# Kernel optimization log

Hardware: AMD Instinct MI355X
Metric: run time of the kernel (lower is better)

Reference implementation:

```python
import jax, jax.numpy as jnp
import numpy as np

B, L, IMG_DIM, D, H = 256, 64, 2048, 1024, 8
DH = D // H
NEG = -1e30
LN_EPS = 1e-5
BN_EPS = 1e-5
RESW = 0.5
K = 2


def setup_inputs() -> dict:
    key = jax.random.key(0)
    ks = jax.random.split(key, 24)
    n = jax.random.normal
    inp = {
        "images": n(ks[0], (B, L, IMG_DIM), dtype=jnp.float32),
        "image_lengths": jax.random.randint(ks[1], (B,), 2, L + 1).astype(jnp.int32),
        # FC_MLP: Linear(2048->512) -> BN -> ReLU -> Linear(512->1024)
        "fc1_w": n(ks[2], (512, IMG_DIM)) * 0.02,
        "fc1_b": jnp.zeros((512,)),
        "bn_g": jnp.ones((512,)),
        "bn_b": jnp.zeros((512,)),
        "bn_m": jnp.zeros((512,)),
        "bn_v": jnp.ones((512,)),
        "fc2_w": n(ks[3], (D, 512)) * 0.02,
        "fc2_b": jnp.zeros((D,)),
        # MHA
        "in_w": n(ks[4], (3 * D, D)) * 0.02,
        "in_b": jnp.zeros((3 * D,)),
        "out_w": n(ks[5], (D, D)) * 0.02,
        "out_b": jnp.zeros((D,)),
        "ln1_g": jnp.ones((D,)),
        "ln1_b": jnp.zeros((D,)),
        # FFN (dim_feedforward = embed_size = 1024)
        "ff1_w": n(ks[6], (D, D)) * 0.02,
        "ff1_b": jnp.zeros((D,)),
        "ff2_w": n(ks[7], (D, D)) * 0.02,
        "ff2_b": jnp.zeros((D,)),
        "ln2_g": jnp.ones((D,)),
        "ln2_b": jnp.zeros((D,)),
    }
    return inp


def _layernorm(x, g, b):
    mu = x.mean(-1, keepdims=True)
    var = ((x - mu) ** 2).mean(-1, keepdims=True)
    return (x - mu) * jax.lax.rsqrt(var + LN_EPS) * g + b


def reference(images, image_lengths, fc1_w, fc1_b, bn_g, bn_b, bn_m, bn_v,
              fc2_w, fc2_b, in_w, in_b, out_w, out_b, ln1_g, ln1_b,
              ff1_w, ff1_b, ff2_w, ff2_b, ln2_g, ln2_b):
    lengths = image_lengths
    valid = jnp.arange(L)[None, :] < lengths[:, None]          # (B, L) True=valid

    # FC_MLP (BN in eval mode with running stats)
    h = images @ fc1_w.T + fc1_b
    h = (h - bn_m) * jax.lax.rsqrt(bn_v + BN_EPS) * bn_g + bn_b
    h = jax.nn.relu(h)
    emb = h @ fc2_w.T + fc2_b                                   # (B, L, D)

    # Maxk_Pooling_Variable: top-k over valid tokens, mean of top-k, per feature
    masked = jnp.where(valid[:, :, None], emb, NEG)             # (B, L, D)
    topk, _ = jax.lax.top_k(masked.transpose(0, 2, 1), K)       # (B, D, K)
    emb_res = topk.mean(-1)                                     # (B, D)

    # TransformerEncoderLayer (post-norm, relu, dropout=0) with key padding mask
    qkv = emb @ in_w.T + in_b
    q, k, v = jnp.split(qkv, 3, axis=-1)
    q = q.reshape(B, L, H, DH)
    k = k.reshape(B, L, H, DH)
    v = v.reshape(B, L, H, DH)
    scores = jnp.einsum("bqhd,bkhd->bhqk", q, k) / np.sqrt(DH)
    scores = scores + jnp.where(valid, 0.0, NEG)[:, None, None, :]
    attn = jax.nn.softmax(scores, axis=-1)
    ctx = jnp.einsum("bhqk,bkhd->bqhd", attn, v).reshape(B, L, D)
    ctx = ctx @ out_w.T + out_b
    x = _layernorm(emb + ctx, ln1_g, ln1_b)
    ff = jax.nn.relu(x @ ff1_w.T + ff1_b) @ ff2_w.T + ff2_b
    x = _layernorm(x + ff, ln2_g, ln2_b)                        # (B, L, D)

    # Avg_Pooling_Variable: mean over first lengths[i] tokens
    avg = (x * valid[:, :, None]).sum(1) / lengths[:, None].astype(x.dtype)

    out = RESW * emb_res + (1.0 - RESW) * avg                   # (B, D)
    norm = jnp.sqrt((out ** 2).sum(-1, keepdims=True)) + 1e-8
    return out / norm
```

## Files before the change

kernel.cpp:

```cpp
#include <hip/hip_runtime.h>
#include <stdint.h>
#include <stddef.h>


typedef short s16x8 __attribute__((ext_vector_type(8)));
typedef short s16x4 __attribute__((ext_vector_type(4)));
typedef float f32x4 __attribute__((ext_vector_type(4)));

#define LN_EPSF 1e-5f
#define BN_EPSF 1e-5f

__device__ __forceinline__ short f2bf(float f) {
  union { float f; uint32_t u; } x; x.f = f;
  uint32_t r = x.u + 0x7fffu + ((x.u >> 16) & 1u);
  return (short)(r >> 16);
}
__device__ __forceinline__ float bf2f(short s) {
  union { uint32_t u; float f; } x; x.u = ((uint32_t)(uint16_t)s) << 16;
  return x.f;
}

typedef const __attribute__((address_space(1))) short glb_s16_t;
typedef __attribute__((address_space(3))) short lds_s16_t;

__device__ __forceinline__ void stage16(const short* g, short* l) {
  __builtin_amdgcn_global_load_lds((glb_s16_t*)g, (lds_s16_t*)l, 16, 0, 0);
}

__device__ __forceinline__ int swz(int off) {
  return off ^ (((off >> 7) & 3) << 4);
}

enum { EPI_PLAIN = 0, EPI_FF1 = 3, EPI_RES = 4 };

__global__ __launch_bounds__(256)
void prefix_kernel(const int* __restrict__ lens, int* __restrict__ cum,
                   int* __restrict__ hdr, int* __restrict__ tokmap) {
  __shared__ int wsum[4];
  __shared__ int sc[256];
  __shared__ int mcpad;
  const int tid = threadIdx.x, lane = tid & 63, wave = tid >> 6;
  const int mylen = lens[tid];
  int v = mylen;
#pragma unroll
  for (int o = 1; o < 64; o <<= 1) {
    int t = __shfl_up(v, o);
    if (lane >= o) v += t;
  }
  if (lane == 63) wsum[wave] = v;
  __syncthreads();
  int add = 0;
#pragma unroll
  for (int w2 = 0; w2 < 4; ++w2) if (w2 < wave) add += wsum[w2];
  const int incl = v + add;
  const int excl = incl - mylen;
  cum[tid] = excl;
  sc[tid] = excl;
  if (tid == 255) {
    hdr[0] = incl;
    mcpad  = (incl + 255) & ~255;
    hdr[1] = mcpad;
  }
  __syncthreads();
  for (int l = 0; l < mylen; ++l) tokmap[excl + l] = tid * 64 + l;
  const int mc = sc[255] + lens[255];
  for (int i = mc + tid; i < mcpad; i += 256) tokmap[i] = 0;
}

struct CvtArgs { const float* src[6]; short* dst[6]; int n4[6]; };

__global__ __launch_bounds__(256)
void cvt_gather_kernel(const float* __restrict__ img,
                       const int* __restrict__ tokmap,
                       const int* __restrict__ hdr, short* __restrict__ out,
                       CvtArgs a) {
  const int n4 = hdr[1] << 9;
  const int stride = gridDim.x * 256;
  for (int i = blockIdx.x * 256 + threadIdx.x; i < n4; i += stride) {
    const int row = i >> 9, col = i & 511;
    float4 v = ((const float4*)img)[(size_t)tokmap[row] * 512 + col];
    s16x4 h; h[0] = f2bf(v.x); h[1] = f2bf(v.y); h[2] = f2bf(v.z); h[3] = f2bf(v.w);
    ((s16x4*)out)[i] = h;
  }
#pragma unroll
  for (int s = 0; s < 6; ++s) {
    const int n = a.n4[s];
    const float4* in = (const float4*)a.src[s];
    s16x4* outp = (s16x4*)a.dst[s];
    for (int i = blockIdx.x * 256 + threadIdx.x; i < n; i += stride) {
      float4 v = in[i];
      s16x4 h; h[0] = f2bf(v.x); h[1] = f2bf(v.y); h[2] = f2bf(v.z); h[3] = f2bf(v.w);
      outp[i] = h;
    }
  }
}

template<int EPI>
__global__ __launch_bounds__(512, 2)
void gemm256(const short* __restrict__ A, const short* __restrict__ Bw,
             const float* __restrict__ bias, const short* __restrict__ res16,
             const int* __restrict__ hdr,
             float* __restrict__ out32, short* __restrict__ out16,
             int M, int N, int K) {
  extern __shared__ char smem[];
  (void)M;
  const int tid  = threadIdx.x;
  const int lane = tid & 63;
  const int w    = tid >> 6;
  const int wr   = w >> 2;
  const int wc   = w & 3;
  const int lrow = lane & 15;
  const int cg   = lane >> 4;
  const int NH   = K >> 5;
  const int gx   = gridDim.x;

  const int p = blockIdx.y * gx + blockIdx.x;
  const int nwork = (hdr[1] >> 8) * gx;
  if (p >= nwork) return;
  const int xcd = p & 7, off = p >> 3;
  const int q = nwork >> 3, r = nwork & 7;
  const int wg = (xcd < r ? xcd * (q + 1) : r * (q + 1) + (xcd - r) * q) + off;
  const int m0 = (wg / gx) * 256;
  const int n0 = (wg % gx) * 256;

  const int ldb = K * 2;
  size_t gA[2], gB[2];
#pragma unroll
  for (int j = 0; j < 2; ++j) {
    const int pp = tid * 16 + j * 8192;
    const int l = swz(pp);
    const int row = l >> 6, colb = l & 63;
    gA[j] = (size_t)(m0 + row) * ldb + colb;
    gB[j] = (size_t)(n0 + row) * ldb + colb;
  }
  const char* Ab = (const char*)A;
  const char* Bb = (const char*)Bw;
  char* ldsA = smem;
  char* ldsB = smem + 65536;
  const int wofs = w * 1024;

  auto stageApart = [&](int i) {
    const int rg = ((i & 3) << 14) + wofs;
    const int ko = i * 64;
    stage16((const short*)(Ab + gA[0] + ko), (short*)(ldsA + rg));
    stage16((const short*)(Ab + gA[1] + ko), (short*)(ldsA + rg + 8192));
  };
  auto stageBpart = [&](int i) {
    const int rg = ((i & 3) << 14) + wofs;
    const int ko = i * 64;
    stage16((const short*)(Bb + gB[0] + ko), (short*)(ldsB + rg));
    stage16((const short*)(Bb + gB[1] + ko), (short*)(ldsB + rg + 8192));
  };

  int offA[8], offB[4];
#pragma unroll
  for (int mf = 0; mf < 8; ++mf)
    offA[mf] = swz((wr * 128 + mf * 16 + lrow) * 64 + cg * 16);
#pragma unroll
  for (int nf = 0; nf < 4; ++nf)
    offB[nf] = swz((wc * 64 + nf * 16 + lrow) * 64 + cg * 16);

  f32x4 acc[8][4] = {};

  stageApart(0); stageBpart(0);
  stageApart(1); stageBpart(1);
  stageApart(2); stageBpart(2);
  asm volatile("s_waitcnt vmcnt(8)" ::: "memory");
  __builtin_amdgcn_s_barrier();
  __builtin_amdgcn_sched_barrier(0);
  s16x8 af_cur[4], bf_cur[4], af_nxt[4], bf_nxt[4], af2[4];
#pragma unroll
  for (int m = 0; m < 4; ++m) af_cur[m] = *(const s16x8*)(ldsA + offA[m]);
#pragma unroll
  for (int n = 0; n < 4; ++n) bf_cur[n] = *(const s16x8*)(ldsB + offB[n]);

  for (int i = 0; i < NH - 1; ++i) {
    const int si  = i & 3;
    const int si1 = (i + 1) & 3;
    const char* pA  = ldsA + (si  << 14);
    const char* pA1 = ldsA + (si1 << 14);
    const char* pB1 = ldsB + (si1 << 14);

    if (i + 2 < NH) { asm volatile("s_waitcnt vmcnt(4)" ::: "memory"); }
    else            { asm volatile("s_waitcnt vmcnt(0)" ::: "memory"); }
    __builtin_amdgcn_s_barrier();
    __builtin_amdgcn_sched_barrier(0);

#pragma unroll
    for (int m = 0; m < 4; ++m) af_nxt[m] = *(const s16x8*)(pA + offA[m + 4]);
#pragma unroll
    for (int n = 0; n < 4; ++n) bf_nxt[n] = *(const s16x8*)(pB1 + offB[n]);
    if (i + 3 < NH) stageApart(i + 3);
    asm volatile("s_waitcnt lgkmcnt(8)" ::: "memory");
    __builtin_amdgcn_sched_barrier(0);
    __builtin_amdgcn_s_setprio(1);
#pragma unroll
    for (int m = 0; m < 4; ++m)
#pragma unroll
      for (int n = 0; n < 4; ++n)
        acc[m][n] = __builtin_amdgcn_mfma_f32_16x16x32_bf16(af_cur[m], bf_cur[n], acc[m][n], 0, 0, 0);
    __builtin_amdgcn_s_setprio(0);

#pragma unroll
    for (int m = 0; m < 4; ++m) af2[m] = *(const s16x8*)(pA1 + offA[m]);
    if (i + 3 < NH) stageBpart(i + 3);
    asm volatile("s_waitcnt lgkmcnt(4)" ::: "memory");
    __builtin_amdgcn_sched_barrier(0);
    __builtin_amdgcn_s_setprio(1);
#pragma unroll
    for (int m = 0; m < 4; ++m)
#pragma unroll
      for (int n = 0; n < 4; ++n)
        acc[m + 4][n] = __builtin_amdgcn_mfma_f32_16x16x32_bf16(af_nxt[m], bf_cur[n], acc[m + 4][n], 0, 0, 0);
    __builtin_amdgcn_s_setprio(0);

#pragma unroll
    for (int m = 0; m < 4; ++m) af_cur[m] = af2[m];
#pragma unroll
    for (int n = 0; n < 4; ++n) bf_cur[n] = bf_nxt[n];
  }

  {
    const char* pA = ldsA + (((NH - 1) & 3) << 14);
    asm volatile("s_waitcnt vmcnt(0)" ::: "memory");
    __builtin_amdgcn_s_barrier();
    __builtin_amdgcn_sched_barrier(0);
#pragma unroll
    for (int m = 0; m < 4; ++m) af_nxt[m] = *(const s16x8*)(pA + offA[m + 4]);
    asm volatile("s_waitcnt lgkmcnt(4)" ::: "memory");
    __builtin_amdgcn_sched_barrier(0);
    __builtin_amdgcn_s_setprio(1);
#pragma unroll
    for (int m = 0; m < 4; ++m)
#pragma unroll
      for (int n = 0; n < 4; ++n)
        acc[m][n] = __builtin_amdgcn_mfma_f32_16x16x32_bf16(af_cur[m], bf_cur[n], acc[m][n], 0, 0, 0);
    __builtin_amdgcn_s_setprio(0);
    asm volatile("s_waitcnt lgkmcnt(0)" ::: "memory");
    __builtin_amdgcn_sched_barrier(0);
    __builtin_amdgcn_s_setprio(1);
#pragma unroll
    for (int m = 0; m < 4; ++m)
#pragma unroll
      for (int n = 0; n < 4; ++n)
        acc[m + 4][n] = __builtin_amdgcn_mfma_f32_16x16x32_bf16(af_nxt[m], bf_cur[n], acc[m + 4][n], 0, 0, 0);
    __builtin_amdgcn_s_setprio(0);
  }

  const int ecol0 = n0 + wc * 64 + lrow;
  float bz[4];
#pragma unroll
  for (int nf = 0; nf < 4; ++nf) bz[nf] = bias[ecol0 + nf * 16];
  const int erow0 = m0 + wr * 128 + (cg << 2);

#pragma unroll
  for (int mf = 0; mf < 8; ++mf) {
#pragma unroll
    for (int nf = 0; nf < 4; ++nf) {
#pragma unroll
      for (int r2 = 0; r2 < 4; ++r2) {
        const int row = erow0 + mf * 16 + r2;
        const size_t idx = (size_t)row * N + (ecol0 + nf * 16);
        const float v = acc[mf][nf][r2] + bz[nf];
        if constexpr (EPI == EPI_PLAIN) {
          out16[idx] = f2bf(v);
        } else if constexpr (EPI == EPI_FF1) {
          out16[idx] = f2bf(fmaxf(v, 0.f));
        } else {
          out32[idx] = v + bf2f(res16[idx]);
        }
      }
    }
  }
}

template<int EPI>
__global__ __launch_bounds__(512, 4)
void gemm128p(const short* __restrict__ A, const short* __restrict__ Bw,
              const float* __restrict__ bias, const short* __restrict__ res16,
              const int* __restrict__ hdr,
              float* __restrict__ out32, short* __restrict__ out16,
              int N, int K) {
  extern __shared__ char smem[];
  const int tid  = threadIdx.x;
  const int lane = tid & 63;
  const int w    = tid >> 6;
  const int wr   = w >> 2;
  const int wc   = w & 3;
  const int lrow = lane & 15;
  const int cg   = lane >> 4;
  const int NH   = K >> 5;
  const int gx   = gridDim.x;

  const int p = blockIdx.y * gx + blockIdx.x;
  const int nwork = (hdr[1] >> 7) * gx;
  if (p >= nwork) return;
  const int xcd = p & 7, off = p >> 3;
  const int q = nwork >> 3, r = nwork & 7;
  const int wg = (xcd < r ? xcd * (q + 1) : r * (q + 1) + (xcd - r) * q) + off;
  const int m0 = (wg / gx) * 128;
  const int n0 = (wg % gx) * 128;

  const int ldb = K * 2;
  size_t gA, gB;
  {
    const int pp = tid * 16;
    const int l = swz(pp);
    const int row = l >> 6, colb = l & 63;
    gA = (size_t)(m0 + row) * ldb + colb;
    gB = (size_t)(n0 + row) * ldb + colb;
  }
  const char* Ab = (const char*)A;
  const char* Bb = (const char*)Bw;
  char* ldsA = smem;
  char* ldsB = smem + 32768;
  const int wofs = w * 1024;

  auto stageA = [&](int i) {
    stage16((const short*)(Ab + gA + i * 64), (short*)(ldsA + ((i & 3) << 13) + wofs));
  };
  auto stageB = [&](int i) {
    stage16((const short*)(Bb + gB + i * 64), (short*)(ldsB + ((i & 3) << 13) + wofs));
  };

  int offA[4], offB[2];
#pragma unroll
  for (int mf = 0; mf < 4; ++mf)
    offA[mf] = swz((wr * 64 + mf * 16 + lrow) * 64 + cg * 16);
#pragma unroll
  for (int nf = 0; nf < 2; ++nf)
    offB[nf] = swz((wc * 32 + nf * 16 + lrow) * 64 + cg * 16);

  f32x4 acc[4][2] = {};

  stageA(0); stageB(0);
  stageA(1); stageB(1);
  stageA(2); stageB(2);
  asm volatile("s_waitcnt vmcnt(4)" ::: "memory");
  __builtin_amdgcn_s_barrier();
  __builtin_amdgcn_sched_barrier(0);
  s16x8 af_cur[2], bf_cur[2], af_nxt[2], bf_nxt[2], af2[2];
#pragma unroll
  for (int m = 0; m < 2; ++m) af_cur[m] = *(const s16x8*)(ldsA + offA[m]);
#pragma unroll
  for (int n = 0; n < 2; ++n) bf_cur[n] = *(const s16x8*)(ldsB + offB[n]);

  for (int i = 0; i < NH - 1; ++i) {
    const char* pA  = ldsA + ((i & 3) << 13);
    const char* pA1 = ldsA + (((i + 1) & 3) << 13);
    const char* pB1 = ldsB + (((i + 1) & 3) << 13);

    if (i + 2 < NH) { asm volatile("s_waitcnt vmcnt(2)" ::: "memory"); }
    else            { asm volatile("s_waitcnt vmcnt(0)" ::: "memory"); }
    __builtin_amdgcn_s_barrier();
    __builtin_amdgcn_sched_barrier(0);

#pragma unroll
    for (int m = 0; m < 2; ++m) af_nxt[m] = *(const s16x8*)(pA + offA[m + 2]);
#pragma unroll
    for (int n = 0; n < 2; ++n) bf_nxt[n] = *(const s16x8*)(pB1 + offB[n]);
    if (i + 3 < NH) stageA(i + 3);
    asm volatile("s_waitcnt lgkmcnt(4)" ::: "memory");
    __builtin_amdgcn_sched_barrier(0);
    __builtin_amdgcn_s_setprio(1);
#pragma unroll
    for (int m = 0; m < 2; ++m)
#pragma unroll
      for (int n = 0; n < 2; ++n)
        acc[m][n] = __builtin_amdgcn_mfma_f32_16x16x32_bf16(af_cur[m], bf_cur[n], acc[m][n], 0, 0, 0);
    __builtin_amdgcn_s_setprio(0);

#pragma unroll
    for (int m = 0; m < 2; ++m) af2[m] = *(const s16x8*)(pA1 + offA[m]);
    if (i + 3 < NH) stageB(i + 3);
    asm volatile("s_waitcnt lgkmcnt(2)" ::: "memory");
    __builtin_amdgcn_sched_barrier(0);
    __builtin_amdgcn_s_setprio(1);
#pragma unroll
    for (int m = 0; m < 2; ++m)
#pragma unroll
      for (int n = 0; n < 2; ++n)
        acc[m + 2][n] = __builtin_amdgcn_mfma_f32_16x16x32_bf16(af_nxt[m], bf_cur[n], acc[m + 2][n], 0, 0, 0);
    __builtin_amdgcn_s_setprio(0);

#pragma unroll
    for (int m = 0; m < 2; ++m) af_cur[m] = af2[m];
#pragma unroll
    for (int n = 0; n < 2; ++n) bf_cur[n] = bf_nxt[n];
  }

  {
    const char* pA = ldsA + (((NH - 1) & 3) << 13);
    asm volatile("s_waitcnt vmcnt(0)" ::: "memory");
    __builtin_amdgcn_s_barrier();
    __builtin_amdgcn_sched_barrier(0);
#pragma unroll
    for (int m = 0; m < 2; ++m) af_nxt[m] = *(const s16x8*)(pA + offA[m + 2]);
    asm volatile("s_waitcnt lgkmcnt(2)" ::: "memory");
    __builtin_amdgcn_sched_barrier(0);
    __builtin_amdgcn_s_setprio(1);
#pragma unroll
    for (int m = 0; m < 2; ++m)
#pragma unroll
      for (int n = 0; n < 2; ++n)
        acc[m][n] = __builtin_amdgcn_mfma_f32_16x16x32_bf16(af_cur[m], bf_cur[n], acc[m][n], 0, 0, 0);
    __builtin_amdgcn_s_setprio(0);
    asm volatile("s_waitcnt lgkmcnt(0)" ::: "memory");
    __builtin_amdgcn_sched_barrier(0);
    __builtin_amdgcn_s_setprio(1);
#pragma unroll
    for (int m = 0; m < 2; ++m)
#pragma unroll
      for (int n = 0; n < 2; ++n)
        acc[m + 2][n] = __builtin_amdgcn_mfma_f32_16x16x32_bf16(af_nxt[m], bf_cur[n], acc[m + 2][n], 0, 0, 0);
    __builtin_amdgcn_s_setprio(0);
  }

  const int ecol0 = n0 + wc * 32 + lrow;
  float bz[2];
#pragma unroll
  for (int nf = 0; nf < 2; ++nf) bz[nf] = bias[ecol0 + nf * 16];
  const int erow0 = m0 + wr * 64 + (cg << 2);

#pragma unroll
  for (int mf = 0; mf < 4; ++mf) {
#pragma unroll
    for (int nf = 0; nf < 2; ++nf) {
#pragma unroll
      for (int r2 = 0; r2 < 4; ++r2) {
        const int row = erow0 + mf * 16 + r2;
        const size_t idx = (size_t)row * N + (ecol0 + nf * 16);
        const float v = acc[mf][nf][r2] + bz[nf];
        if constexpr (EPI == EPI_PLAIN) {
          out16[idx] = f2bf(v);
        } else if constexpr (EPI == EPI_FF1) {
          out16[idx] = f2bf(fmaxf(v, 0.f));
        } else {
          out32[idx] = v + bf2f(res16[idx]);
        }
      }
    }
  }
}

__global__ __launch_bounds__(256)
void gemm_bt_h1(const short* __restrict__ A, const short* __restrict__ Bw,
                const float* __restrict__ bias,
                const float* __restrict__ bn_g, const float* __restrict__ bn_b,
                const float* __restrict__ bn_m, const float* __restrict__ bn_v,
                const int* __restrict__ hdr,
                short* __restrict__ out16, int M, int N, int K) {
  __shared__ short As[128 * 32];
  __shared__ short Bs[128 * 32];
  (void)M;
  const int m0 = blockIdx.y * 128;
  if (m0 >= hdr[1]) return;
  const int tid  = threadIdx.x;
  const int lane = tid & 63;
  const int wave = tid >> 6;
  const int n0 = blockIdx.x * 128;
  const int wm = (wave >> 1) * 64;
  const int wn = (wave & 1) * 64;
  const int lrow = lane & 15;
  const int lk8  = (lane >> 4) * 8;

  f32x4 acc[4][4] = {};

  const int srow = wave * 16 + (lane >> 2);
  const int scol = (lane & 3) * 8;
  const short* gA = A  + (size_t)(m0 + srow) * K + scol;
  const short* gB = Bw + (size_t)(n0 + srow) * K + scol;
  short* lA = &As[(wave * 16) * 32];
  short* lB = &Bs[(wave * 16) * 32];
  const size_t half = (size_t)64 * K;

  for (int k0 = 0; k0 < K; k0 += 32) {
    stage16(gA + k0,        lA);
    stage16(gA + half + k0, lA + 64 * 32);
    stage16(gB + k0,        lB);
    stage16(gB + half + k0, lB + 64 * 32);
    __syncthreads();
    s16x8 af[4], bfr[4];
#pragma unroll
    for (int m = 0; m < 4; ++m)
      af[m] = *(const s16x8*)&As[(wm + m * 16 + lrow) * 32 + lk8];
#pragma unroll
    for (int n = 0; n < 4; ++n)
      bfr[n] = *(const s16x8*)&Bs[(wn + n * 16 + lrow) * 32 + lk8];
#pragma unroll
    for (int m = 0; m < 4; ++m)
#pragma unroll
      for (int n = 0; n < 4; ++n)
        acc[m][n] = __builtin_amdgcn_mfma_f32_16x16x32_bf16(af[m], bfr[n], acc[m][n], 0, 0, 0);
    __syncthreads();
  }

  const int erow = m0 + wm + ((lane >> 4) << 2);
  const int ecol = n0 + wn + lrow;
  float sc[4], sh[4];
#pragma unroll
  for (int n = 0; n < 4; ++n) {
    const int c = ecol + n * 16;
    const float s = bn_g[c] * rsqrtf(bn_v[c] + BN_EPSF);
    sc[n] = s;
    sh[n] = (bias[c] - bn_m[c]) * s + bn_b[c];
  }
#pragma unroll
  for (int m = 0; m < 4; ++m)
#pragma unroll
    for (int n = 0; n < 4; ++n)
#pragma unroll
      for (int r = 0; r < 4; ++r) {
        const size_t idx = (size_t)(erow + m * 16 + r) * N + (ecol + n * 16);
        out16[idx] = f2bf(fmaxf(acc[m][n][r] * sc[n] + sh[n], 0.f));
      }
}

__global__ __launch_bounds__(256)
void topk_kernel(const short* __restrict__ emb16, const int* __restrict__ lens,
                 const int* __restrict__ cum, float* __restrict__ er) {
  const int b = blockIdx.x;
  const int len = lens[b];
  const size_t base = (size_t)cum[b] * 1024;
  const int tid = threadIdx.x;
#pragma unroll
  for (int j = 0; j < 4; ++j) {
    const int d = j * 256 + tid;
    float m1 = -3.0e38f, m2 = -3.0e38f;
    for (int l = 0; l < len; ++l) {
      const float v = bf2f(emb16[base + (size_t)l * 1024 + d]);
      if (v > m1) { m2 = m1; m1 = v; }
      else        { m2 = fmaxf(m2, v); }
    }
    er[(size_t)b * 1024 + d] = 0.5f * (m1 + m2);
  }
}

__global__ __launch_bounds__(256)
void attn_kernel(const short* __restrict__ qkv, const int* __restrict__ lens,
                 const int* __restrict__ cum, short* __restrict__ ctx) {
  __shared__ short Qs[64 * 128];
  __shared__ short Ks[64 * 128];
  __shared__ short Vt[128 * 64];
  const int tid  = threadIdx.x;
  const int lane = tid & 63;
  const int wave = tid >> 6;
  const int b = blockIdx.x >> 3;
  const int h = blockIdx.x & 7;
  const int len = lens[b];
  const int rb  = cum[b];
  const size_t qb = (size_t)rb * 3072 + h * 128;

  {
    const int rr = wave * 4 + (lane >> 4);
    const int cc = (lane & 15) * 8;
#pragma unroll
    for (int r = 0; r < 4; ++r) {
      stage16(qkv + qb +        (size_t)(r * 16 + rr) * 3072 + cc, &Qs[(r * 16 + wave * 4) * 128]);
      stage16(qkv + qb + 1024 + (size_t)(r * 16 + rr) * 3072 + cc, &Ks[(r * 16 + wave * 4) * 128]);
    }
  }
#pragma unroll
  for (int i = 0; i < 2; ++i) {
    const int c  = i * 256 + tid;
    const int lp = c >> 4;
    const int dg = c & 15;
    const short* src = qkv + qb + 2048 + (size_t)(2 * lp) * 3072 + dg * 8;
    s16x8 v0 = *(const s16x8*)src;
    s16x8 v1 = *(const s16x8*)(src + 3072);
    const bool ok0 = (2 * lp)     < len;
    const bool ok1 = (2 * lp + 1) < len;
#pragma unroll
    for (int j = 0; j < 8; ++j) {
      const uint32_t lo = ok0 ? (uint32_t)(uint16_t)v0[j] : 0u;
      const uint32_t hi = ok1 ? (uint32_t)(uint16_t)v1[j] : 0u;
      *(uint32_t*)&Vt[(dg * 8 + j) * 64 + 2 * lp] = lo | (hi << 16);
    }
  }
  __syncthreads();

  const int lrow = lane & 15;
  const int lk8  = (lane >> 4) * 8;

  f32x4 sacc[4] = {};
#pragma unroll
  for (int ks = 0; ks < 4; ++ks) {
    s16x8 aq = *(const s16x8*)&Qs[(wave * 16 + lrow) * 128 + ks * 32 + lk8];
#pragma unroll
    for (int n = 0; n < 4; ++n) {
      s16x8 bk = *(const s16x8*)&Ks[(n * 16 + lrow) * 128 + ks * 32 + lk8];
      sacc[n] = __builtin_amdgcn_mfma_f32_16x16x32_bf16(aq, bk, sacc[n], 0, 0, 0);
    }
  }

  const float scale = 0.08838834764831845f;
#pragma unroll
  for (int r = 0; r < 4; ++r) {
    float sv[4];
    float mx = -1e30f;
#pragma unroll
    for (int n = 0; n < 4; ++n) {
      float v = sacc[n][r] * scale;
      if (n * 16 + lrow >= len) v = -1e30f;
      sv[n] = v;
      mx = fmaxf(mx, v);
    }
    mx = fmaxf(mx, __shfl_xor(mx, 1));
    mx = fmaxf(mx, __shfl_xor(mx, 2));
    mx = fmaxf(mx, __shfl_xor(mx, 4));
    mx = fmaxf(mx, __shfl_xor(mx, 8));
    float pv[4], sum = 0.f;
#pragma unroll
    for (int n = 0; n < 4; ++n) { pv[n] = __expf(sv[n] - mx); sum += pv[n]; }
    sum += __shfl_xor(sum, 1);
    sum += __shfl_xor(sum, 2);
    sum += __shfl_xor(sum, 4);
    sum += __shfl_xor(sum, 8);
    const float inv = 1.f / sum;
    const int prow = wave * 16 + ((lane >> 4) << 2) + r;
#pragma unroll
    for (int n = 0; n < 4; ++n)
      Qs[prow * 128 + n * 16 + lrow] = f2bf(pv[n] * inv);
  }
  __syncthreads();

  f32x4 oacc[8] = {};
#pragma unroll
  for (int ks = 0; ks < 2; ++ks) {
    s16x8 ap = *(const s16x8*)&Qs[(wave * 16 + lrow) * 128 + ks * 32 + lk8];
#pragma unroll
    for (int n = 0; n < 8; ++n) {
      s16x8 bv = *(const s16x8*)&Vt[(n * 16 + lrow) * 64 + ks * 32 + lk8];
      oacc[n] = __builtin_amdgcn_mfma_f32_16x16x32_bf16(ap, bv, oacc[n], 0, 0, 0);
    }
  }
  const size_t ob = (size_t)rb * 1024 + h * 128;
#pragma unroll
  for (int n = 0; n < 8; ++n)
#pragma unroll
    for (int r = 0; r < 4; ++r) {
      const int row = wave * 16 + ((lane >> 4) << 2) + r;
      if (row < len)
        ctx[ob + (size_t)row * 1024 + n * 16 + lrow] = f2bf(oacc[n][r]);
    }
}

__global__ __launch_bounds__(256)
void ln_kernel(const float* __restrict__ x, const float* __restrict__ gg,
               const float* __restrict__ bb, const int* __restrict__ hdr,
               short* __restrict__ y16) {
  if ((int)blockIdx.x >= hdr[1]) return;
  __shared__ float red[8];
  const int tid = threadIdx.x;
  const int lane = tid & 63;
  const int wave = tid >> 6;
  const size_t base = (size_t)blockIdx.x * 1024;
  float4 v = ((const float4*)(x + base))[tid];
  float s1 = v.x + v.y + v.z + v.w;
  float s2 = v.x * v.x + v.y * v.y + v.z * v.z + v.w * v.w;
#pragma unroll
  for (int o = 1; o < 64; o <<= 1) { s1 += __shfl_xor(s1, o); s2 += __shfl_xor(s2, o); }
  if (lane == 0) { red[wave] = s1; red[wave + 4] = s2; }
  __syncthreads();
  s1 = red[0] + red[1] + red[2] + red[3];
  s2 = red[4] + red[5] + red[6] + red[7];
  const float mu  = s1 * (1.f / 1024.f);
  const float var = fmaxf(s2 * (1.f / 1024.f) - mu * mu, 0.f);
  const float rs  = rsqrtf(var + LN_EPSF);
  float4 g4 = ((const float4*)gg)[tid];
  float4 b4 = ((const float4*)bb)[tid];
  s16x4 hh;
  hh[0] = f2bf((v.x - mu) * rs * g4.x + b4.x);
  hh[1] = f2bf((v.y - mu) * rs * g4.y + b4.y);
  hh[2] = f2bf((v.z - mu) * rs * g4.z + b4.z);
  hh[3] = f2bf((v.w - mu) * rs * g4.w + b4.w);
  ((s16x4*)(y16 + base))[tid] = hh;
}

__global__ __launch_bounds__(256)
void ln2_final_kernel(const float* __restrict__ x, const float* __restrict__ gg,
                      const float* __restrict__ bb, const float* __restrict__ er,
                      const int* __restrict__ lens, const int* __restrict__ cum,
                      float* __restrict__ out) {
  __shared__ float part[4][1024];
  __shared__ float red[4];
  const int tid = threadIdx.x, lane = tid & 63, w = tid >> 6;
  const int b = blockIdx.x, len = lens[b];
  const size_t rb = (size_t)cum[b];
  float4 g4[4], b4[4];
#pragma unroll
  for (int k = 0; k < 4; ++k) {
    g4[k] = ((const float4*)gg)[k * 64 + lane];
    b4[k] = ((const float4*)bb)[k * 64 + lane];
  }
  float4 acc[4];
#pragma unroll
  for (int k = 0; k < 4; ++k) acc[k] = make_float4(0.f, 0.f, 0.f, 0.f);

  for (int l = w; l < len; l += 4) {
    const float4* row = (const float4*)(x + (rb + l) * 1024);
    float4 v[4]; float s1 = 0.f, s2 = 0.f;
#pragma unroll
    for (int k = 0; k < 4; ++k) {
      v[k] = row[k * 64 + lane];
      s1 += v[k].x + v[k].y + v[k].z + v[k].w;
      s2 += v[k].x * v[k].x + v[k].y * v[k].y + v[k].z * v[k].z + v[k].w * v[k].w;
    }
#pragma unroll
    for (int o = 1; o < 64; o <<= 1) { s1 += __shfl_xor(s1, o); s2 += __shfl_xor(s2, o); }
    const float mu = s1 * (1.f / 1024.f);
    const float rs = rsqrtf(fmaxf(s2 * (1.f / 1024.f) - mu * mu, 0.f) + LN_EPSF);
#pragma unroll
    for (int k = 0; k < 4; ++k) {
      acc[k].x += (v[k].x - mu) * rs * g4[k].x + b4[k].x;
      acc[k].y += (v[k].y - mu) * rs * g4[k].y + b4[k].y;
      acc[k].z += (v[k].z - mu) * rs * g4[k].z + b4[k].z;
      acc[k].w += (v[k].w - mu) * rs * g4[k].w + b4[k].w;
    }
  }
#pragma unroll
  for (int k = 0; k < 4; ++k)
    ((float4*)&part[w][0])[k * 64 + lane] = acc[k];
  __syncthreads();

  float4 s = ((const float4*)&part[0][0])[tid];
#pragma unroll
  for (int w2 = 1; w2 < 4; ++w2) {
    float4 t4 = ((const float4*)&part[0][0])[w2 * 256 + tid];
    s.x += t4.x; s.y += t4.y; s.z += t4.z; s.w += t4.w;
  }
  const float il = 0.5f / (float)len;
  float4 e = ((const float4*)(er + (size_t)b * 1024))[tid];
  const float o0 = 0.5f * e.x + s.x * il;
  const float o1 = 0.5f * e.y + s.y * il;
  const float o2 = 0.5f * e.z + s.z * il;
  const float o3 = 0.5f * e.w + s.w * il;
  float ss = o0 * o0 + o1 * o1 + o2 * o2 + o3 * o3;
#pragma unroll
  for (int o = 1; o < 64; o <<= 1) ss += __shfl_xor(ss, o);
  if (lane == 0) red[w] = ss;
  __syncthreads();
  ss = red[0] + red[1] + red[2] + red[3];
  const float nrm = 1.f / (sqrtf(ss) + 1e-8f);
  ((float4*)(out + (size_t)b * 1024))[tid] = make_float4(o0 * nrm, o1 * nrm, o2 * nrm, o3 * nrm);
}

extern "C" void kernel_launch(void* const* d_in, const int* in_sizes, int n_in,
                              void* d_out, int out_size, void* d_ws, size_t ws_size,
                              hipStream_t stream) {
  (void)in_sizes; (void)n_in; (void)out_size; (void)ws_size;
  const float* images = (const float*)d_in[0];
  const int*   lens   = (const int*)d_in[1];
  const float* fc1_w = (const float*)d_in[2];
  const float* fc1_b = (const float*)d_in[3];
  const float* bn_g  = (const float*)d_in[4];
  const float* bn_b  = (const float*)d_in[5];
  const float* bn_m  = (const float*)d_in[6];
  const float* bn_v  = (const float*)d_in[7];
  const float* fc2_w = (const float*)d_in[8];
  const float* fc2_b = (const float*)d_in[9];
  const float* in_w  = (const float*)d_in[10];
  const float* in_b  = (const float*)d_in[11];
  const float* out_w = (const float*)d_in[12];
  const float* out_b = (const float*)d_in[13];
  const float* ln1_g = (const float*)d_in[14];
  const float* ln1_b = (const float*)d_in[15];
  const float* ff1_w = (const float*)d_in[16];
  const float* ff1_b = (const float*)d_in[17];
  const float* ff2_w = (const float*)d_in[18];
  const float* ff2_b = (const float*)d_in[19];
  const float* ln2_g = (const float*)d_in[20];
  const float* ln2_b = (const float*)d_in[21];
  float* out = (float*)d_out;

  char* ws = (char*)d_ws;
  const size_t OFF_IMG16 = 0;
  const size_t OFF_FC1W  = 67108864;
  const size_t OFF_FC2W  = OFF_FC1W + 2097152;
  const size_t OFF_INW   = OFF_FC2W + 1048576;
  const size_t OFF_OUTW  = OFF_INW  + 6291456;
  const size_t OFF_FF1W  = OFF_OUTW + 2097152;
  const size_t OFF_FF2W  = OFF_FF1W + 2097152;
  const size_t OFF_H1    = OFF_FF2W + 2097152;
  const size_t OFF_EMB16 = OFF_H1 + 16777216;
  const size_t OFF_QKV   = OFF_EMB16 + 33554432;
  const size_t OFF_CTX   = OFF_QKV + 101056512;
  const size_t OFF_ERES  = OFF_CTX + 33554432;
  const size_t OFF_HDR   = OFF_ERES + 1048576;
  const size_t OFF_CUM   = OFF_HDR + 256;
  const size_t OFF_TOK   = OFF_CUM + 1024;

  short* img16  = (short*)(ws + OFF_IMG16);
  short* fc1w16 = (short*)(ws + OFF_FC1W);
  short* fc2w16 = (short*)(ws + OFF_FC2W);
  short* inw16  = (short*)(ws + OFF_INW);
  short* outw16 = (short*)(ws + OFF_OUTW);
  short* ff1w16 = (short*)(ws + OFF_FF1W);
  short* ff2w16 = (short*)(ws + OFF_FF2W);
  short* h1     = (short*)(ws + OFF_H1);
  short* emb16  = (short*)(ws + OFF_EMB16);
  short* qkv16  = (short*)(ws + OFF_QKV);
  short* ctx16  = (short*)(ws + OFF_CTX);
  float* embres = (float*)(ws + OFF_ERES);
  int*   hdr    = (int*)(ws + OFF_HDR);
  int*   cum    = (int*)(ws + OFF_CUM);
  int*   tokmap = (int*)(ws + OFF_TOK);
  float* x1s = (float*)(ws + OFF_IMG16);
  short* x1h = emb16;
  short* ffh = ctx16;
  float* x2s = (float*)(ws + OFF_IMG16);

  const dim3 blk(256);
  const size_t SMEM256 = 131072;
  const size_t SMEM128 = 65536;

  prefix_kernel<<<1, blk, 0, stream>>>(lens, cum, hdr, tokmap);

  CvtArgs ca;
  ca.src[0] = fc1_w; ca.dst[0] = fc1w16; ca.n4[0] = 1048576 / 4;
  ca.src[1] = fc2_w; ca.dst[1] = fc2w16; ca.n4[1] = 524288 / 4;
  ca.src[2] = in_w;  ca.dst[2] = inw16;  ca.n4[2] = 3145728 / 4;
  ca.src[3] = out_w; ca.dst[3] = outw16; ca.n4[3] = 1048576 / 4;
  ca.src[4] = ff1_w; ca.dst[4] = ff1w16; ca.n4[4] = 1048576 / 4;
  ca.src[5] = ff2_w; ca.dst[5] = ff2w16; ca.n4[5] = 1048576 / 4;
  cvt_gather_kernel<<<2048, blk, 0, stream>>>(images, tokmap, hdr, img16, ca);

  gemm_bt_h1<<<dim3(4, 128), blk, 0, stream>>>(
      img16, fc1w16, fc1_b, bn_g, bn_b, bn_m, bn_v, hdr, h1, 16384, 512, 2048);
  gemm128p<EPI_PLAIN><<<dim3(8, 128), 512, SMEM128, stream>>>(
      h1, fc2w16, fc2_b, nullptr, hdr, nullptr, emb16, 1024, 512);
  topk_kernel<<<256, blk, 0, stream>>>(emb16, lens, cum, embres);
  gemm256<EPI_PLAIN><<<dim3(12, 64), 512, SMEM256, stream>>>(
      emb16, inw16, in_b, nullptr, hdr, nullptr, qkv16, 16384, 3072, 1024);
  attn_kernel<<<2048, blk, 0, stream>>>(qkv16, lens, cum, ctx16);
  gemm128p<EPI_RES><<<dim3(8, 128), 512, SMEM128, stream>>>(
      ctx16, outw16, out_b, emb16, hdr, x1s, nullptr, 1024, 1024);
  ln_kernel<<<16384, blk, 0, stream>>>(x1s, ln1_g, ln1_b, hdr, x1h);
  gemm128p<EPI_FF1><<<dim3(8, 128), 512, SMEM128, stream>>>(
      x1h, ff1w16, ff1_b, nullptr, hdr, nullptr, ffh, 1024, 1024);
  gemm128p<EPI_RES><<<dim3(8, 128), 512, SMEM128, stream>>>(
      ffh, ff2w16, ff2_b, x1h, hdr, x2s, nullptr, 1024, 1024);
  ln2_final_kernel<<<256, blk, 0, stream>>>(x2s, ln2_g, ln2_b, embres, lens, cum, out);
}
```

Before: 398.3 us.

## Route fc1 through pipelined GEMM and store residual sums as bf16

Replaces the simple single-buffered fc1 GEMM with the pipelined 128-tile gemm128p kernel, adding a BN+ReLU epilogue variant. Residual-add outputs before both layernorms are now written as bf16 instead of fp32, and the LN kernels read bf16, which halves that traffic. The cost is lower precision in the pre-LN sums.

```diff
diff --git a/kernel.cpp b/kernel.cpp
--- a/kernel.cpp
+++ b/kernel.cpp
@@ -31,7 +31,7 @@
   return off ^ (((off >> 7) & 3) << 4);
 }
 
-enum { EPI_PLAIN = 0, EPI_FF1 = 3, EPI_RES = 4 };
+enum { EPI_PLAIN = 0, EPI_FF1 = 3, EPI_RES = 4, EPI_H1 = 5 };
 
 __global__ __launch_bounds__(256)
 void prefix_kernel(const int* __restrict__ lens, int* __restrict__ cum,
@@ -98,12 +98,9 @@
 template<int EPI>
 __global__ __launch_bounds__(512, 2)
 void gemm256(const short* __restrict__ A, const short* __restrict__ Bw,
-             const float* __restrict__ bias, const short* __restrict__ res16,
-             const int* __restrict__ hdr,
-             float* __restrict__ out32, short* __restrict__ out16,
-             int M, int N, int K) {
+             const float* __restrict__ bias, const int* __restrict__ hdr,
+             short* __restrict__ out16, int N, int K) {
   extern __shared__ char smem[];
-  (void)M;
   const int tid  = threadIdx.x;
   const int lane = tid & 63;
   const int w    = tid >> 6;
@@ -254,32 +251,24 @@
   const int erow0 = m0 + wr * 128 + (cg << 2);
 
 #pragma unroll
-  for (int mf = 0; mf < 8; ++mf) {
-#pragma unroll
-    for (int nf = 0; nf < 4; ++nf) {
+  for (int mf = 0; mf < 8; ++mf)
+#pragma unroll
+    for (int nf = 0; nf < 4; ++nf)
 #pragma unroll
       for (int r2 = 0; r2 < 4; ++r2) {
         const int row = erow0 + mf * 16 + r2;
         const size_t idx = (size_t)row * N + (ecol0 + nf * 16);
-        const float v = acc[mf][nf][r2] + bz[nf];
-        if constexpr (EPI == EPI_PLAIN) {
-          out16[idx] = f2bf(v);
-        } else if constexpr (EPI == EPI_FF1) {
-          out16[idx] = f2bf(fmaxf(v, 0.f));
-        } else {
-          out32[idx] = v + bf2f(res16[idx]);
-        }
+        out16[idx] = f2bf(acc[mf][nf][r2] + bz[nf]);
       }
-    }
-  }
 }
 
 template<int EPI>
 __global__ __launch_bounds__(512, 4)
 void gemm128p(const short* __restrict__ A, const short* __restrict__ Bw,
               const float* __restrict__ bias, const short* __restrict__ res16,
-              const int* __restrict__ hdr,
-              float* __restrict__ out32, short* __restrict__ out16,
+              const float* __restrict__ bnG, const float* __restrict__ bnB,
+              const float* __restrict__ bnM, const float* __restrict__ bnV,
+              const int* __restrict__ hdr, short* __restrict__ out16,
               int N, int K) {
   extern __shared__ char smem[];
   const int tid  = threadIdx.x;
@@ -417,10 +406,20 @@
   }
 
   const int ecol0 = n0 + wc * 32 + lrow;
-  float bz[2];
-#pragma unroll
-  for (int nf = 0; nf < 2; ++nf) bz[nf] = bias[ecol0 + nf * 16];
   const int erow0 = m0 + wr * 64 + (cg << 2);
+  float bz[2], sc[2], sh[2];
+#pragma unroll
+  for (int nf = 0; nf < 2; ++nf) {
+    const int c = ecol0 + nf * 16;
+    if constexpr (EPI == EPI_H1) {
+      const float s = bnG[c] * rsqrtf(bnV[c] + BN_EPSF);
+      sc[nf] = s;
+      sh[nf] = (bias[c] - bnM[c]) * s + bnB[c];
+    } else {
+      bz[nf] = bias[c];
+    }
+  }
+  (void)bnG; (void)bnB; (void)bnM; (void)bnV;
 
 #pragma unroll
   for (int mf = 0; mf < 4; ++mf) {
@@ -430,90 +429,21 @@
       for (int r2 = 0; r2 < 4; ++r2) {
         const int row = erow0 + mf * 16 + r2;
         const size_t idx = (size_t)row * N + (ecol0 + nf * 16);
-        const float v = acc[mf][nf][r2] + bz[nf];
-        if constexpr (EPI == EPI_PLAIN) {
-          out16[idx] = f2bf(v);
-        } else if constexpr (EPI == EPI_FF1) {
-          out16[idx] = f2bf(fmaxf(v, 0.f));
+        if constexpr (EPI == EPI_H1) {
+          out16[idx] = f2bf(fmaxf(acc[mf][nf][r2] * sc[nf] + sh[nf], 0.f));
         } else {
-          out32[idx] = v + bf2f(res16[idx]);
+          const float v = acc[mf][nf][r2] + bz[nf];
+          if constexpr (EPI == EPI_PLAIN) {
+            out16[idx] = f2bf(v);
+          } else if constexpr (EPI == EPI_FF1) {
+            out16[idx] = f2bf(fmaxf(v, 0.f));
+          } else {
+            out16[idx] = f2bf(v + bf2f(res16[idx]));
+          }
         }
       }
     }
   }
-}
-
-__global__ __launch_bounds__(256)
-void gemm_bt_h1(const short* __restrict__ A, const short* __restrict__ Bw,
-                const float* __restrict__ bias,
-                const float* __restrict__ bn_g, const float* __restrict__ bn_b,
-                const float* __restrict__ bn_m, const float* __restrict__ bn_v,
-                const int* __restrict__ hdr,
-                short* __restrict__ out16, int M, int N, int K) {
-  __shared__ short As[128 * 32];
-  __shared__ short Bs[128 * 32];
-  (void)M;
-  const int m0 = blockIdx.y * 128;
-  if (m0 >= hdr[1]) return;
-  const int tid  = threadIdx.x;
-  const int lane = tid & 63;
-  const int wave = tid >> 6;
-  const int n0 = blockIdx.x * 128;
-  const int wm = (wave >> 1) * 64;
-  const int wn = (wave & 1) * 64;
-  const int lrow = lane & 15;
-  const int lk8  = (lane >> 4) * 8;
-
-  f32x4 acc[4][4] = {};
-
-  const int srow = wave * 16 + (lane >> 2);
-  const int scol = (lane & 3) * 8;
-  const short* gA = A  + (size_t)(m0 + srow) * K + scol;
-  const short* gB = Bw + (size_t)(n0 + srow) * K + scol;
-  short* lA = &As[(wave * 16) * 32];
-  short* lB = &Bs[(wave * 16) * 32];
-  const size_t half = (size_t)64 * K;
-
-  for (int k0 = 0; k0 < K; k0 += 32) {
-    stage16(gA + k0,        lA);
-    stage16(gA + half + k0, lA + 64 * 32);
-    stage16(gB + k0,        lB);
-    stage16(gB + half + k0, lB + 64 * 32);
-    __syncthreads();
-    s16x8 af[4], bfr[4];
-#pragma unroll
-    for (int m = 0; m < 4; ++m)
-      af[m] = *(const s16x8*)&As[(wm + m * 16 + lrow) * 32 + lk8];
-#pragma unroll
-    for (int n = 0; n < 4; ++n)
-      bfr[n] = *(const s16x8*)&Bs[(wn + n * 16 + lrow) * 32 + lk8];
-#pragma unroll
-    for (int m = 0; m < 4; ++m)
-#pragma unroll
-      for (int n = 0; n < 4; ++n)
-        acc[m][n] = __builtin_amdgcn_mfma_f32_16x16x32_bf16(af[m], bfr[n], acc[m][n], 0, 0, 0);
-    __syncthreads();
-  }
-
-  const int erow = m0 + wm + ((lane >> 4) << 2);
-  const int ecol = n0 + wn + lrow;
-  float sc[4], sh[4];
-#pragma unroll
-  for (int n = 0; n < 4; ++n) {
-    const int c = ecol + n * 16;
-    const float s = bn_g[c] * rsqrtf(bn_v[c] + BN_EPSF);
-    sc[n] = s;
-    sh[n] = (bias[c] - bn_m[c]) * s + bn_b[c];
-  }
-#pragma unroll
-  for (int m = 0; m < 4; ++m)
-#pragma unroll
-    for (int n = 0; n < 4; ++n)
-#pragma unroll
-      for (int r = 0; r < 4; ++r) {
-        const size_t idx = (size_t)(erow + m * 16 + r) * N + (ecol + n * 16);
-        out16[idx] = f2bf(fmaxf(acc[m][n][r] * sc[n] + sh[n], 0.f));
-      }
 }
 
 __global__ __launch_bounds__(256)
@@ -646,7 +576,7 @@
 }
 
 __global__ __launch_bounds__(256)
-void ln_kernel(const float* __restrict__ x, const float* __restrict__ gg,
+void ln_kernel(const short* __restrict__ x16, const float* __restrict__ gg,
                const float* __restrict__ bb, const int* __restrict__ hdr,
                short* __restrict__ y16) {
   if ((int)blockIdx.x >= hdr[1]) return;
@@ -655,9 +585,10 @@
   const int lane = tid & 63;
   const int wave = tid >> 6;
   const size_t base = (size_t)blockIdx.x * 1024;
-  float4 v = ((const float4*)(x + base))[tid];
-  float s1 = v.x + v.y + v.z + v.w;
-  float s2 = v.x * v.x + v.y * v.y + v.z * v.z + v.w * v.w;
+  s16x4 hv = ((const s16x4*)(x16 + base))[tid];
+  const float v0 = bf2f(hv[0]), v1 = bf2f(hv[1]), v2 = bf2f(hv[2]), v3 = bf2f(hv[3]);
+  float s1 = v0 + v1 + v2 + v3;
+  float s2 = v0 * v0 + v1 * v1 + v2 * v2 + v3 * v3;
 #pragma unroll
   for (int o = 1; o < 64; o <<= 1) { s1 += __shfl_xor(s1, o); s2 += __shfl_xor(s2, o); }
   if (lane == 0) { red[wave] = s1; red[wave + 4] = s2; }
@@ -670,15 +601,15 @@
   float4 g4 = ((const float4*)gg)[tid];
   float4 b4 = ((const float4*)bb)[tid];
   s16x4 hh;
-  hh[0] = f2bf((v.x - mu) * rs * g4.x + b4.x);
-  hh[1] = f2bf((v.y - mu) * rs * g4.y + b4.y);
-  hh[2] = f2bf((v.z - mu) * rs * g4.z + b4.z);
-  hh[3] = f2bf((v.w - mu) * rs * g4.w + b4.w);
+  hh[0] = f2bf((v0 - mu) * rs * g4.x + b4.x);
+  hh[1] = f2bf((v1 - mu) * rs * g4.y + b4.y);
+  hh[2] = f2bf((v2 - mu) * rs * g4.z + b4.z);
+  hh[3] = f2bf((v3 - mu) * rs * g4.w + b4.w);
   ((s16x4*)(y16 + base))[tid] = hh;
 }
 
 __global__ __launch_bounds__(256)
-void ln2_final_kernel(const float* __restrict__ x, const float* __restrict__ gg,
+void ln2_final_kernel(const short* __restrict__ x16, const float* __restrict__ gg,
                       const float* __restrict__ bb, const float* __restrict__ er,
                       const int* __restrict__ lens, const int* __restrict__ cum,
                       float* __restrict__ out) {
@@ -698,11 +629,12 @@
   for (int k = 0; k < 4; ++k) acc[k] = make_float4(0.f, 0.f, 0.f, 0.f);
 
   for (int l = w; l < len; l += 4) {
-    const float4* row = (const float4*)(x + (rb + l) * 1024);
+    const s16x4* row = (const s16x4*)(x16 + (rb + l) * 1024);
     float4 v[4]; float s1 = 0.f, s2 = 0.f;
 #pragma unroll
     for (int k = 0; k < 4; ++k) {
-      v[k] = row[k * 64 + lane];
+      s16x4 hv = row[k * 64 + lane];
+      v[k] = make_float4(bf2f(hv[0]), bf2f(hv[1]), bf2f(hv[2]), bf2f(hv[3]));
       s1 += v[k].x + v[k].y + v[k].z + v[k].w;
       s2 += v[k].x * v[k].x + v[k].y * v[k].y + v[k].z * v[k].z + v[k].w * v[k].w;
     }
@@ -805,10 +737,10 @@
   int*   hdr    = (int*)(ws + OFF_HDR);
   int*   cum    = (int*)(ws + OFF_CUM);
   int*   tokmap = (int*)(ws + OFF_TOK);
-  float* x1s = (float*)(ws + OFF_IMG16);
-  short* x1h = emb16;
-  short* ffh = ctx16;
-  float* x2s = (float*)(ws + OFF_IMG16);
+  short* x1sum = (short*)(ws + OFF_IMG16);
+  short* x1h   = emb16;
+  short* ffh   = ctx16;
+  short* x2sum = (short*)(ws + OFF_IMG16);
 
   const dim3 blk(256);
   const size_t SMEM256 = 131072;
@@ -825,20 +757,20 @@
   ca.src[5] = ff2_w; ca.dst[5] = ff2w16; ca.n4[5] = 1048576 / 4;
   cvt_gather_kernel<<<2048, blk, 0, stream>>>(images, tokmap, hdr, img16, ca);
 
-  gemm_bt_h1<<<dim3(4, 128), blk, 0, stream>>>(
-      img16, fc1w16, fc1_b, bn_g, bn_b, bn_m, bn_v, hdr, h1, 16384, 512, 2048);
+  gemm128p<EPI_H1><<<dim3(4, 128), 512, SMEM128, stream>>>(
+      img16, fc1w16, fc1_b, nullptr, bn_g, bn_b, bn_m, bn_v, hdr, h1, 512, 2048);
   gemm128p<EPI_PLAIN><<<dim3(8, 128), 512, SMEM128, stream>>>(
-      h1, fc2w16, fc2_b, nullptr, hdr, nullptr, emb16, 1024, 512);
+      h1, fc2w16, fc2_b, nullptr, nullptr, nullptr, nullptr, nullptr, hdr, emb16, 1024, 512);
   topk_kernel<<<256, blk, 0, stream>>>(emb16, lens, cum, embres);
   gemm256<EPI_PLAIN><<<dim3(12, 64), 512, SMEM256, stream>>>(
-      emb16, inw16, in_b, nullptr, hdr, nullptr, qkv16, 16384, 3072, 1024);
+      emb16, inw16, in_b, hdr, qkv16, 3072, 1024);
   attn_kernel<<<2048, blk, 0, stream>>>(qkv16, lens, cum, ctx16);
   gemm128p<EPI_RES><<<dim3(8, 128), 512, SMEM128, stream>>>(
-      ctx16, outw16, out_b, emb16, hdr, x1s, nullptr, 1024, 1024);
-  ln_kernel<<<16384, blk, 0, stream>>>(x1s, ln1_g, ln1_b, hdr, x1h);
+      ctx16, outw16, out_b, emb16, nullptr, nullptr, nullptr, nullptr, hdr, x1sum, 1024, 1024);
+  ln_kernel<<<16384, blk, 0, stream>>>(x1sum, ln1_g, ln1_b, hdr, x1h);
   gemm128p<EPI_FF1><<<dim3(8, 128), 512, SMEM128, stream>>>(
-      x1h, ff1w16, ff1_b, nullptr, hdr, nullptr, ffh, 1024, 1024);
+      x1h, ff1w16, ff1_b, nullptr, nullptr, nullptr, nullptr, nullptr, hdr, ffh, 1024, 1024);
   gemm128p<EPI_RES><<<dim3(8, 128), 512, SMEM128, stream>>>(
-      ffh, ff2w16, ff2_b, x1h, hdr, x2s, nullptr, 1024, 1024);
-  ln2_final_kernel<<<256, blk, 0, stream>>>(x2s, ln2_g, ln2_b, embres, lens, cum, out);
-}
+      ffh, ff2w16, ff2_b, x1h, nullptr, nullptr, nullptr, nullptr, hdr, x2sum, 1024, 1024);
+  ln2_final_kernel<<<256, blk, 0, stream>>>(x2sum, ln2_g, ln2_b, embres, lens, cum, out);
+}
```

After: 378.7 us. 1.05x faster.
